# Kernel tuning notes

Measured on AMD Instinct MI355X. Metric: run time of the kernel, lower is better.

## Reference

```python
import jax, jax.numpy as jnp
import numpy as np

V = 30000
Y = 30000
D = 768
B = 8
N = 512
PAD_ID = 0
POS_EXPONENT = 1
NEG_INF = 1e12
LN_EPS = 1e-5


def setup_inputs() -> dict:
    key = jax.random.key(0)
    k1, k2, k3, k4, k5 = jax.random.split(key, 5)
    M_s = jax.random.randint(k1, (B, N), 0, V, dtype=jnp.int64)
    E_v = jax.random.normal(k2, (V, D), dtype=jnp.float32) * 0.02
    E_y = jax.random.normal(k3, (Y, D), dtype=jnp.float32) * 0.02
    # padding_idx=0 -> zero rows
    E_v = E_v.at[PAD_ID].set(0.0)
    E_y = E_y.at[PAD_ID].set(0.0)
    W_A = jax.random.normal(k4, (D, D), dtype=jnp.float32) * (1.0 / np.sqrt(D))
    W_O = jax.random.normal(k5, (D, D), dtype=jnp.float32) * (1.0 / np.sqrt(D))
    gamma = jnp.ones((D,), dtype=jnp.float32)
    beta = jnp.zeros((D,), dtype=jnp.float32)
    return {"M_s": M_s, "E_v": E_v, "E_y": E_y, "W_A": W_A, "W_O": W_O,
            "gamma": gamma, "beta": beta}


def positional_rep(seq_len: int, exponent: int) -> jnp.ndarray:
    idx = jnp.arange(seq_len)
    rel = (idx[None, :] - idx[:, None]).astype(jnp.float32)  # [N, N], j - i
    sign = jnp.where(rel >= 0, 1.0, -1.0)
    return sign * jnp.abs(rel) ** exponent


def layer_norm(x, gamma, beta):
    mu = jnp.mean(x, axis=-1, keepdims=True)
    var = jnp.mean((x - mu) ** 2, axis=-1, keepdims=True)
    return (x - mu) * jax.lax.rsqrt(var + LN_EPS) * gamma + beta


def reference(M_s, E_v, E_y, W_A, W_O, gamma, beta):
    # Embedding lookup (dropout is identity at eval / p=0)
    X = E_v[M_s]                                   # [B, N, D]
    Q = X                                          # self-attention mode (v_q=None)
    mask = (M_s != PAD_ID)                         # [B, N]

    # attention: logits = (Q @ W_A) @ X^T + pos_bias, mask, softmax
    logits = jnp.einsum('bnd,bmd->bnm', Q @ W_A, X)  # [B, N, N]
    logits = logits + positional_rep(X.shape[1], POS_EXPONENT)[None]
    logits = jnp.where(mask[:, None, :], logits, -NEG_INF)
    A = jax.nn.softmax(logits, axis=-1)            # [B, N, N]
    Q_c = jnp.einsum('bnm,bmd->bnd', A, X @ W_O)   # [B, N, D]

    H = layer_norm(Q_c + Q, gamma, beta)           # [B, N, D]
    y_logits = jnp.einsum('bnd,yd->bny', H, E_y)   # [B, N, Y]
    return y_logits, A
```

## Files before the change

kernel.cpp:

```cpp
#include <hip/hip_runtime.h>
#include <hip/hip_bf16.h>

using bf16 = __hip_bfloat16;
typedef __attribute__((ext_vector_type(8))) short bf16x8;
typedef __attribute__((ext_vector_type(4))) float f32x4;

#define DEV __device__ __forceinline__

#define AS1 __attribute__((address_space(1)))
#define AS3 __attribute__((address_space(3)))
#define SB  __builtin_amdgcn_sched_barrier(0)
#define BARR __builtin_amdgcn_s_barrier()
#define LG0 asm volatile("s_waitcnt lgkmcnt(0)" ::: "memory")
#define VM4 asm volatile("s_waitcnt vmcnt(4)" ::: "memory")
#define VM0 asm volatile("s_waitcnt vmcnt(0)" ::: "memory")
#define VM48 asm volatile("s_waitcnt vmcnt(48)" ::: "memory")

static constexpr int Bsz = 8, Nseq = 512, Dm = 768, Vv = 30000, Yv = 30000;
static constexpr int Ypad = 30208;
static constexpr int NTILE = 118;
static constexpr int TT = 16 * NTILE;
static constexpr int Tok = Bsz * Nseq;
static constexpr int NT = Dm / 64;

#define MF16(MQ, NQ, BR)                                                      \
    __builtin_amdgcn_s_setprio(1);                                            \
    _Pragma("unroll") for (int mm = 0; mm < 4; ++mm)                          \
    _Pragma("unroll") for (int nn = 0; nn < 2; ++nn) {                        \
        acc[(MQ)*4+mm][(NQ)*2+nn] = __builtin_amdgcn_mfma_f32_16x16x32_bf16(  \
            afr[mm][0], BR[nn][0], acc[(MQ)*4+mm][(NQ)*2+nn], 0, 0, 0);       \
        acc[(MQ)*4+mm][(NQ)*2+nn] = __builtin_amdgcn_mfma_f32_16x16x32_bf16(  \
            afr[mm][1], BR[nn][1], acc[(MQ)*4+mm][(NQ)*2+nn], 0, 0, 0);       \
    }                                                                         \
    __builtin_amdgcn_s_setprio(0);

__global__ __launch_bounds__(512, 2)
void gemm_big(const bf16* __restrict__ Ag, const bf16* __restrict__ Bg,
              float* __restrict__ Cg, float* __restrict__ dump)
{
    __shared__ bf16 sm[8][8192];

    const int p = blockIdx.x;
    const int tid  = threadIdx.x;
    const int lane = tid & 63;
    const int wid  = tid >> 6;
    const int wm   = wid >> 2;
    const int wn   = wid & 3;

    const int lr = tid >> 3;
    const int sc = ((tid & 7) ^ (lr & 7)) << 3;
    const int ldsOff = wid << 9;

    const int fl = lane & 15;
    const int fh = lane >> 4;
    const int e0 = (fh ^ (fl & 7)) << 3;
    const int aro = (wm * 64 + fl) * 64;
    const int bro = (wn * 32 + fl) * 64;

    bf16x8 afr[4][2], b0r[2][2], b1r[2][2];
    f32x4 acc[8][4] = {};
    float* dmp = dump + (size_t)p * 512 + tid;

#define STAGEP(AP, BP, CI, OP, H, TILE)                                        \
    {                                                                          \
        const bf16* _s = ((OP) ? (BP) : (AP)) + (long)(H) * 128 * Dm + (TILE) * 64;\
        __builtin_amdgcn_global_load_lds((const AS1 void*)_s,                  \
            (AS3 void*)&sm[CI][ldsOff], 16, 0, 0);                             \
        __builtin_amdgcn_global_load_lds((const AS1 void*)(_s + (long)64 * Dm),\
            (AS3 void*)&sm[CI][4096 + ldsOff], 16, 0, 0);                      \
    }
#define STAGE(CI, OP, H, TILE) STAGEP(aS, bS, CI, OP, H, TILE)
#define RDA(CI)                                                                \
    _Pragma("unroll") for (int mm = 0; mm < 4; ++mm) {                         \
        afr[mm][0] = *(const bf16x8*)&sm[CI][aro + mm * 1024 + e0];            \
        afr[mm][1] = *(const bf16x8*)&sm[CI][aro + mm * 1024 + (e0 ^ 32)];     \
    }
#define RDB(BR, CI)                                                            \
    _Pragma("unroll") for (int nn = 0; nn < 2; ++nn) {                         \
        BR[nn][0] = *(const bf16x8*)&sm[CI][bro + nn * 1024 + e0];             \
        BR[nn][1] = *(const bf16x8*)&sm[CI][bro + nn * 1024 + (e0 ^ 32)];      \
    }

    int l = p;
    int s0 = (l & 7) * (TT >> 3) + (l >> 3);
    int mT = s0 & 15, nT = s0 >> 4;
    const bf16* aS = Ag + (long)(mT * 256 + lr) * Dm + sc;
    const bf16* bS = Bg + (long)(nT * 256 + lr) * Dm + sc;

    STAGE(0, 0, 0, 0) STAGE(2, 1, 0, 0) STAGE(3, 1, 1, 0) STAGE(1, 0, 1, 0)
    STAGE(4, 0, 0, 1) STAGE(7, 1, 1, 1)
    VM4; SB; BARR; SB;

#pragma unroll 1
    while (true) {
#pragma unroll 1
        for (int t = 0; t < NT - 2; t += 2) {
            STAGE(6, 1, 0, t + 1)
            RDA(0) RDB(b0r, 2)
            SB; BARR; LG0; SB;
            MF16(0, 0, b0r)
            SB; BARR; SB;
            STAGE(5, 0, 1, t + 1)
            RDB(b1r, 3)
            SB; BARR; LG0; SB;
            MF16(0, 1, b1r)
            SB; BARR; SB;
            STAGE(0, 0, 0, t + 2)
            RDA(1)
            SB; BARR; LG0; SB;
            MF16(1, 1, b1r)
            SB; BARR; SB;
            STAGE(3, 1, 1, t + 2)
            VM4; SB; BARR; SB;
            MF16(1, 0, b0r)
            SB; BARR; SB;
            STAGE(2, 1, 0, t + 2)
            RDA(4) RDB(b0r, 6)
            SB; BARR; LG0; SB;
            MF16(0, 0, b0r)
            SB; BARR; SB;
            STAGE(1, 0, 1, t + 2)
            RDB(b1r, 7)
            SB; BARR; LG0; SB;
            MF16(0, 1, b1r)
            SB; BARR; SB;
            STAGE(4, 0, 0, t + 3)
            RDA(5)
            SB; BARR; LG0; SB;
            MF16(1, 1, b1r)
            SB; BARR; SB;
            STAGE(7, 1, 1, t + 3)
            VM4; SB; BARR; SB;
            MF16(1, 0, b0r)
            SB; BARR; SB;
        }

        {
            const int t = NT - 2;
            STAGE(6, 1, 0, t + 1)
            RDA(0) RDB(b0r, 2)
            SB; BARR; LG0; SB;
            MF16(0, 0, b0r)
            SB; BARR; SB;
            STAGE(5, 0, 1, t + 1)
            RDB(b1r, 3)
            SB; BARR; LG0; SB;
            MF16(0, 1, b1r)
            SB; BARR; SB;
            RDA(1)
            SB; BARR; LG0; SB;
            MF16(1, 1, b1r)
            SB; BARR; SB;
            VM0; SB; BARR; SB;
            MF16(1, 0, b0r)
            SB; BARR; SB;
            RDA(4) RDB(b0r, 6)
            SB; BARR; LG0; SB;
            MF16(0, 0, b0r)
            SB; BARR; SB;
            RDB(b1r, 7)
            SB; BARR; LG0; SB;
            MF16(0, 1, b1r)
            SB; BARR; SB;
            RDA(5)
            SB; BARR; LG0; SB;
            MF16(1, 1, b1r)
            SB; BARR; SB;
            MF16(1, 0, b0r)
        }

        const int l2 = l + 256;
        const bool more = (l2 < TT);
        const int s2 = ((l2 & 7) * (TT >> 3) + (l2 >> 3));
        const int mT2 = s2 & 15, nT2 = s2 >> 4;
        const bf16* aS2 = Ag + (long)(mT2 * 256 + lr) * Dm + sc;
        const bf16* bS2 = Bg + (long)(nT2 * 256 + lr) * Dm + sc;
        if (more) {
            STAGEP(aS2, bS2, 0, 0, 0, 0) STAGEP(aS2, bS2, 2, 1, 0, 0)
            STAGEP(aS2, bS2, 3, 1, 1, 0) STAGEP(aS2, bS2, 1, 0, 1, 0)
            STAGEP(aS2, bS2, 4, 0, 0, 1) STAGEP(aS2, bS2, 7, 1, 1, 1)
            SB;
        }
        {
            const int rB = mT * 256 + wm * 64 + fh * 4;
            const int cB = nT * 256 + wn * 32 + fl;
#pragma unroll
            for (int mq = 0; mq < 2; ++mq)
#pragma unroll
            for (int mm = 0; mm < 4; ++mm)
#pragma unroll
            for (int nq = 0; nq < 2; ++nq)
#pragma unroll
            for (int nn = 0; nn < 2; ++nn) {
                const int c = cB + nq * 128 + nn * 16;
                const int r = rB + mq * 128 + mm * 16;
                const bool ok = (c < Yv);
#pragma unroll
                for (int j = 0; j < 4; ++j) {
                    float* dst = ok ? (Cg + (long)(r + j) * Yv + c) : dmp;
                    *dst = acc[mq * 4 + mm][nq * 2 + nn][j];
                }
            }
        }
#pragma unroll
        for (int i = 0; i < 8; ++i)
#pragma unroll
            for (int n = 0; n < 4; ++n) acc[i][n] = (f32x4){0.f, 0.f, 0.f, 0.f};
        if (!more) break;
        l = l2; mT = mT2; nT = nT2; aS = aS2; bS = bS2;
        SB; VM48; SB; BARR; SB;
    }
#undef STAGEP
#undef STAGE
#undef RDA
#undef RDB
}

template<bool STORE_BF16>
__global__ __launch_bounds__(256)
void gemm_bt(const bf16* __restrict__ Ag, const bf16* __restrict__ Bg,
             void* __restrict__ Cg, int M, int Nc, int K, int lda, int ldc,
             long sA, long sB, long sC)
{
    __shared__ bf16 As[128 * 32];
    __shared__ bf16 Bs[128 * 32];

    const int bz = blockIdx.z;
    const bf16* A  = Ag + (long)bz * sA;
    const bf16* Bm = Bg + (long)bz * sB;

    const int bid = blockIdx.x;
    const int nTilesM = M >> 7;
    const int mTile = bid % nTilesM;
    const int nTile = bid / nTilesM;

    const int tid  = threadIdx.x;
    const int wave = tid >> 6;
    const int lane = tid & 63;

    const int sRow = (wave << 4) + (lane >> 2);
    const int sCol = (lane & 3) << 3;

    const long aBase = (long)(mTile * 128) * lda;
    const long bBase = (long)(nTile * 128) * K;

    const int fl = lane & 15;
    const int fh = lane >> 4;
    const int wRow = (wave >> 1) << 6;
    const int wCol = (wave & 1) << 6;

    f32x4 acc[4][4] = {};

    for (int k0 = 0; k0 < K; k0 += 32) {
#pragma unroll
        for (int t = 0; t < 2; ++t) {
            const bf16* gA = A  + aBase + (long)(t * 64 + sRow) * lda + (k0 + sCol);
            const bf16* gB = Bm + bBase + (long)(t * 64 + sRow) * K + (k0 + sCol);
            bf16* lA = &As[(t * 64 + (wave << 4)) * 32];
            bf16* lB = &Bs[(t * 64 + (wave << 4)) * 32];
            __builtin_amdgcn_global_load_lds(
                (const AS1 void*)gA, (AS3 void*)lA, 16, 0, 0);
            __builtin_amdgcn_global_load_lds(
                (const AS1 void*)gB, (AS3 void*)lB, 16, 0, 0);
        }
        __syncthreads();

        bf16x8 af[4], bfg[4];
#pragma unroll
        for (int m = 0; m < 4; ++m)
            af[m] = *(const bf16x8*)&As[(wRow + m * 16 + fl) * 32 + fh * 8];
#pragma unroll
        for (int n = 0; n < 4; ++n)
            bfg[n] = *(const bf16x8*)&Bs[(wCol + n * 16 + fl) * 32 + fh * 8];
#pragma unroll
        for (int m = 0; m < 4; ++m)
#pragma unroll
            for (int n = 0; n < 4; ++n)
                acc[m][n] = __builtin_amdgcn_mfma_f32_16x16x32_bf16(
                    af[m], bfg[n], acc[m][n], 0, 0, 0);
        __syncthreads();
    }

    const int rBase = mTile * 128 + wRow + fh * 4;
    const int cBase = nTile * 128 + wCol + fl;
#pragma unroll
    for (int m = 0; m < 4; ++m) {
#pragma unroll
        for (int n = 0; n < 4; ++n) {
            int gc = cBase + n * 16;
            int gr = rBase + m * 16;
            if (STORE_BF16) {
                bf16* C = (bf16*)Cg + (long)bz * sC;
#pragma unroll
                for (int j = 0; j < 4; ++j)
                    C[(long)(gr + j) * ldc + gc] = __float2bfloat16(acc[m][n][j]);
            } else {
                float* C = (float*)Cg + (long)bz * sC;
#pragma unroll
                for (int j = 0; j < 4; ++j)
                    C[(long)(gr + j) * ldc + gc] = acc[m][n][j];
            }
        }
    }
}

__global__ __launch_bounds__(192) void k_cvt_ey(const float* __restrict__ Ey,
                                                bf16* __restrict__ Eyb)
{
    int row = blockIdx.x;
    int d = threadIdx.x * 4;
    union { bf16 h[4]; uint2 u; } pk;
    if (row < Yv) {
        float4 v = *(const float4*)(Ey + (long)row * Dm + d);
        pk.h[0] = __float2bfloat16(v.x); pk.h[1] = __float2bfloat16(v.y);
        pk.h[2] = __float2bfloat16(v.z); pk.h[3] = __float2bfloat16(v.w);
    } else {
        pk.h[0] = pk.h[1] = pk.h[2] = pk.h[3] = __float2bfloat16(0.f);
    }
    *(uint2*)(Eyb + (long)row * Dm + d) = pk.u;
}

__global__ void k_wT(const float* __restrict__ WA, const float* __restrict__ WO,
                     bf16* __restrict__ Wcat)
{
    __shared__ float t[32][33];
    const float* W = blockIdx.z ? WO : WA;
    bf16* WT = Wcat + (size_t)blockIdx.z * Dm * Dm;
    int bx = blockIdx.x * 32;
    int by = blockIdx.y * 32;
    int tx = threadIdx.x, ty = threadIdx.y;
#pragma unroll
    for (int i = 0; i < 32; i += 8)
        t[ty + i][tx] = W[(long)(bx + ty + i) * Dm + (by + tx)];
    __syncthreads();
#pragma unroll
    for (int i = 0; i < 32; i += 8)
        WT[(long)(by + ty + i) * Dm + (bx + tx)] = __float2bfloat16(t[tx][ty + i]);
}

__global__ __launch_bounds__(192) void k_gather(const int* __restrict__ Ms,
                                                const float* __restrict__ Ev,
                                                bf16* __restrict__ Xb)
{
    int token = blockIdx.x;
    int id = Ms[token];
    int d = threadIdx.x * 4;
    float4 v = *(const float4*)(Ev + (long)id * Dm + d);
    union { bf16 h[4]; uint2 u; } pk;
    pk.h[0] = __float2bfloat16(v.x); pk.h[1] = __float2bfloat16(v.y);
    pk.h[2] = __float2bfloat16(v.z); pk.h[3] = __float2bfloat16(v.w);
    *(uint2*)(Xb + (long)token * Dm + d) = pk.u;
}

__global__ void k_xwoT(const bf16* __restrict__ Xo, bf16* __restrict__ XoT)
{
    __shared__ bf16 t[32][33];
    int b = blockIdx.z;
    const bf16* src = Xo + (long)b * Nseq * 1536 + 768;
    bf16* dst = XoT + (long)b * Dm * Nseq;
    int bx = blockIdx.x * 32;
    int by = blockIdx.y * 32;
    int tx = threadIdx.x, ty = threadIdx.y;
#pragma unroll
    for (int i = 0; i < 32; i += 8)
        t[ty + i][tx] = src[(long)(bx + ty + i) * 1536 + (by + tx)];
    __syncthreads();
#pragma unroll
    for (int i = 0; i < 32; i += 8)
        dst[(long)(by + ty + i) * Nseq + (bx + tx)] = t[tx][ty + i];
}

DEV float waveMax(float v) {
#pragma unroll
    for (int o = 32; o > 0; o >>= 1) v = fmaxf(v, __shfl_xor(v, o, 64));
    return v;
}
DEV float waveSum(float v) {
#pragma unroll
    for (int o = 32; o > 0; o >>= 1) v += __shfl_xor(v, o, 64);
    return v;
}

__global__ __launch_bounds__(256) void k_softmax(const float* __restrict__ L,
                                                 const int* __restrict__ Ms,
                                                 float* __restrict__ Aout,
                                                 bf16* __restrict__ Ab)
{
    __shared__ float red[8];
    int row = blockIdx.x;
    int b = row >> 9, i = row & 511;
    const float* l = L + (long)row * Nseq;
    const int* ms = Ms + (b << 9);
    int t = threadIdx.x;
    int wid = t >> 6, lane = t & 63;
    int j0 = t, j1 = t + 256;

    float a0 = l[j0] + (float)(j0 - i);
    float a1 = l[j1] + (float)(j1 - i);
    if (ms[j0] == 0) a0 = -1e12f;
    if (ms[j1] == 0) a1 = -1e12f;

    float m = waveMax(fmaxf(a0, a1));
    if (lane == 0) red[wid] = m;
    __syncthreads();
    m = fmaxf(fmaxf(red[0], red[1]), fmaxf(red[2], red[3]));

    float e0 = expf(a0 - m), e1 = expf(a1 - m);
    float s = waveSum(e0 + e1);
    if (lane == 0) red[4 + wid] = s;
    __syncthreads();
    s = red[4] + red[5] + red[6] + red[7];
    float inv = 1.0f / s;

    float r0 = e0 * inv, r1 = e1 * inv;
    Aout[(long)row * Nseq + j0] = r0;
    Aout[(long)row * Nseq + j1] = r1;
    Ab[(long)row * Nseq + j0] = __float2bfloat16(r0);
    Ab[(long)row * Nseq + j1] = __float2bfloat16(r1);
}

__global__ __launch_bounds__(256) void k_ln(const float* __restrict__ Qc,
                                            const int* __restrict__ Ms,
                                            const float* __restrict__ Ev,
                                            const float* __restrict__ gamma,
                                            const float* __restrict__ beta,
                                            bf16* __restrict__ Hb)
{
    __shared__ float red[8];
    int row = blockIdx.x;
    int id = Ms[row];
    const float* q = Qc + (long)row * Dm;
    const float* e = Ev + (long)id * Dm;
    int t = threadIdx.x;
    int wid = t >> 6, lane = t & 63;

    float x[3];
#pragma unroll
    for (int c = 0; c < 3; ++c) x[c] = q[t + c * 256] + e[t + c * 256];

    float s = waveSum(x[0] + x[1] + x[2]);
    if (lane == 0) red[wid] = s;
    __syncthreads();
    float mu = (red[0] + red[1] + red[2] + red[3]) * (1.0f / 768.0f);

    float vs = 0.f;
#pragma unroll
    for (int c = 0; c < 3; ++c) { float d = x[c] - mu; vs += d * d; }
    vs = waveSum(vs);
    if (lane == 0) red[4 + wid] = vs;
    __syncthreads();
    float var = (red[4] + red[5] + red[6] + red[7]) * (1.0f / 768.0f);
    float rstd = rsqrtf(var + 1e-5f);

#pragma unroll
    for (int c = 0; c < 3; ++c) {
        int d = t + c * 256;
        Hb[(long)row * Dm + d] =
            __float2bfloat16((x[c] - mu) * rstd * gamma[d] + beta[d]);
    }
}

extern "C" void kernel_launch(void* const* d_in, const int* in_sizes, int n_in,
                              void* d_out, int out_size, void* d_ws, size_t ws_size,
                              hipStream_t stream)
{
    const int*   Ms    = (const int*)d_in[0];
    const float* Ev    = (const float*)d_in[1];
    const float* Ey    = (const float*)d_in[2];
    const float* WA    = (const float*)d_in[3];
    const float* WO    = (const float*)d_in[4];
    const float* gamma = (const float*)d_in[5];
    const float* beta  = (const float*)d_in[6];

    float* y_out = (float*)d_out;
    float* A_out = y_out + (size_t)Tok * Yv;

    char* ws = (char*)d_ws;
    size_t off = 0;
    auto alloc = [&](size_t n) { char* p = ws + off; off += (n + 255) & ~(size_t)255; return p; };
    bf16*  Xb    = (bf16*) alloc((size_t)Tok * Dm * 2);
    bf16*  WcatT = (bf16*) alloc((size_t)2 * Dm * Dm * 2);
    bf16*  QXWb  = (bf16*) alloc((size_t)Tok * 1536 * 2);
    bf16*  XWobT = (bf16*) alloc((size_t)Tok * Dm * 2);
    float* Lf    = (float*)alloc((size_t)Tok * Nseq * 4);
    bf16*  Ab    = (bf16*) alloc((size_t)Tok * Nseq * 2);
    float* Qc    = (float*)alloc((size_t)Tok * Dm * 4);
    bf16*  Hb    = (bf16*) alloc((size_t)Tok * Dm * 2);
    bf16*  Eyb   = (bf16*) alloc((size_t)Ypad * Dm * 2);
    float* dump  = (float*)alloc((size_t)256 * 512 * 4);

    k_cvt_ey<<<dim3(Ypad), dim3(192), 0, stream>>>(Ey, Eyb);
    k_wT<<<dim3(24, 24, 2), dim3(32, 8), 0, stream>>>(WA, WO, WcatT);
    k_gather<<<dim3(Tok), dim3(192), 0, stream>>>(Ms, Ev, Xb);
    gemm_bt<true><<<dim3(384), dim3(256), 0, stream>>>(
        Xb, WcatT, (void*)QXWb, Tok, 1536, Dm, Dm, 1536, 0L, 0L, 0L);
    gemm_bt<false><<<dim3(16, 1, 8), dim3(256), 0, stream>>>(
        QXWb, Xb, (void*)Lf, Nseq, Nseq, Dm, 1536, Nseq,
        (long)Nseq * 1536, (long)Nseq * Dm, (long)Nseq * Nseq);
    k_softmax<<<dim3(Tok), dim3(256), 0, stream>>>(Lf, Ms, A_out, Ab);
    k_xwoT<<<dim3(16, 24, 8), dim3(32, 8), 0, stream>>>(QXWb, XWobT);
    gemm_bt<false><<<dim3(24, 1, 8), dim3(256), 0, stream>>>(
        Ab, XWobT, (void*)Qc, Nseq, Dm, Nseq, Nseq, Dm,
        (long)Nseq * Nseq, (long)Dm * Nseq, (long)Nseq * Dm);
    k_ln<<<dim3(Tok), dim3(256), 0, stream>>>(Qc, Ms, Ev, gamma, beta, Hb);
    gemm_big<<<dim3(256), dim3(512), 0, stream>>>(Hb, Eyb, y_out, dump);
}
```

Before: 397.9 us.

## Pin A-tile per block in big GEMM, use nontemporal stores, widen Ey conversion

The persistent output GEMM now walks tiles so that each block keeps a fixed M tile (mT constant) and only advances along N. This lets it keep reusing the same A-row addresses and drop the A pointer recomputation. Output logits and softmax probabilities are written with nontemporal stores so the large streaming writes do not evict cached operands. The E_y fp32-to-bf16 conversion kernel now processes 8 elements per thread with nontemporal loads and 16-byte stores over a flat index. The new tile walk changes L2 reuse patterns across blocks and relies on TT being divisible so every block sees the same mT.

```diff
diff --git a/kernel.cpp b/kernel.cpp
--- a/kernel.cpp
+++ b/kernel.cpp
@@ -81,9 +81,9 @@
         BR[nn][1] = *(const bf16x8*)&sm[CI][bro + nn * 1024 + (e0 ^ 32)];      \
     }
 
-    int l = p;
-    int s0 = (l & 7) * (TT >> 3) + (l >> 3);
-    int mT = s0 & 15, nT = s0 >> 4;
+    int s = (p & 7) * 32 + (p >> 3);
+    const int mT = s & 15;
+    int nT = s >> 4;
     const bf16* aS = Ag + (long)(mT * 256 + lr) * Dm + sc;
     const bf16* bS = Bg + (long)(nT * 256 + lr) * Dm + sc;
 
@@ -169,16 +169,14 @@
             MF16(1, 0, b0r)
         }
 
-        const int l2 = l + 256;
-        const bool more = (l2 < TT);
-        const int s2 = ((l2 & 7) * (TT >> 3) + (l2 >> 3));
-        const int mT2 = s2 & 15, nT2 = s2 >> 4;
-        const bf16* aS2 = Ag + (long)(mT2 * 256 + lr) * Dm + sc;
+        const int s2 = s + 256;
+        const bool more = (s2 < TT);
+        const int nT2 = s2 >> 4;
         const bf16* bS2 = Bg + (long)(nT2 * 256 + lr) * Dm + sc;
         if (more) {
-            STAGEP(aS2, bS2, 0, 0, 0, 0) STAGEP(aS2, bS2, 2, 1, 0, 0)
-            STAGEP(aS2, bS2, 3, 1, 1, 0) STAGEP(aS2, bS2, 1, 0, 1, 0)
-            STAGEP(aS2, bS2, 4, 0, 0, 1) STAGEP(aS2, bS2, 7, 1, 1, 1)
+            STAGEP(aS, bS2, 0, 0, 0, 0) STAGEP(aS, bS2, 2, 1, 0, 0)
+            STAGEP(aS, bS2, 3, 1, 1, 0) STAGEP(aS, bS2, 1, 0, 1, 0)
+            STAGEP(aS, bS2, 4, 0, 0, 1) STAGEP(aS, bS2, 7, 1, 1, 1)
             SB;
         }
         {
@@ -198,7 +196,7 @@
 #pragma unroll
                 for (int j = 0; j < 4; ++j) {
                     float* dst = ok ? (Cg + (long)(r + j) * Yv + c) : dmp;
-                    *dst = acc[mq * 4 + mm][nq * 2 + nn][j];
+                    __builtin_nontemporal_store(acc[mq * 4 + mm][nq * 2 + nn][j], dst);
                 }
             }
         }
@@ -207,7 +205,7 @@
 #pragma unroll
             for (int n = 0; n < 4; ++n) acc[i][n] = (f32x4){0.f, 0.f, 0.f, 0.f};
         if (!more) break;
-        l = l2; mT = mT2; nT = nT2; aS = aS2; bS = bS2;
+        s = s2; nT = nT2; bS = bS2;
         SB; VM48; SB; BARR; SB;
     }
 #undef STAGEP
@@ -304,20 +302,26 @@
     }
 }
 
-__global__ __launch_bounds__(192) void k_cvt_ey(const float* __restrict__ Ey,
+__global__ __launch_bounds__(256) void k_cvt_ey(const float* __restrict__ Ey,
                                                 bf16* __restrict__ Eyb)
 {
-    int row = blockIdx.x;
-    int d = threadIdx.x * 4;
-    union { bf16 h[4]; uint2 u; } pk;
+    const long idx = ((long)blockIdx.x * 256 + threadIdx.x) * 8;
+    const int row = (int)(idx / Dm);
+    union { bf16 h[8]; uint4 u; } pk;
     if (row < Yv) {
-        float4 v = *(const float4*)(Ey + (long)row * Dm + d);
-        pk.h[0] = __float2bfloat16(v.x); pk.h[1] = __float2bfloat16(v.y);
-        pk.h[2] = __float2bfloat16(v.z); pk.h[3] = __float2bfloat16(v.w);
+        const f32x4* s = (const f32x4*)(Ey + idx);
+        f32x4 a = __builtin_nontemporal_load(s);
+        f32x4 b = __builtin_nontemporal_load(s + 1);
+#pragma unroll
+        for (int i = 0; i < 4; ++i) {
+            pk.h[i]     = __float2bfloat16(a[i]);
+            pk.h[4 + i] = __float2bfloat16(b[i]);
+        }
     } else {
-        pk.h[0] = pk.h[1] = pk.h[2] = pk.h[3] = __float2bfloat16(0.f);
-    }
-    *(uint2*)(Eyb + (long)row * Dm + d) = pk.u;
+#pragma unroll
+        for (int i = 0; i < 8; ++i) pk.h[i] = __float2bfloat16(0.f);
+    }
+    *(uint4*)(Eyb + idx) = pk.u;
 }
 
 __global__ void k_wT(const float* __restrict__ WA, const float* __restrict__ WO,
@@ -413,8 +417,8 @@
     float inv = 1.0f / s;
 
     float r0 = e0 * inv, r1 = e1 * inv;
-    Aout[(long)row * Nseq + j0] = r0;
-    Aout[(long)row * Nseq + j1] = r1;
+    __builtin_nontemporal_store(r0, &Aout[(long)row * Nseq + j0]);
+    __builtin_nontemporal_store(r1, &Aout[(long)row * Nseq + j1]);
     Ab[(long)row * Nseq + j0] = __float2bfloat16(r0);
     Ab[(long)row * Nseq + j1] = __float2bfloat16(r1);
 }
@@ -489,7 +493,7 @@
     bf16*  Eyb   = (bf16*) alloc((size_t)Ypad * Dm * 2);
     float* dump  = (float*)alloc((size_t)256 * 512 * 4);
 
-    k_cvt_ey<<<dim3(Ypad), dim3(192), 0, stream>>>(Ey, Eyb);
+    k_cvt_ey<<<dim3(11328), dim3(256), 0, stream>>>(Ey, Eyb);
     k_wT<<<dim3(24, 24, 2), dim3(32, 8), 0, stream>>>(WA, WO, WcatT);
     k_gather<<<dim3(Tok), dim3(192), 0, stream>>>(Ms, Ev, Xb);
     gemm_bt<true><<<dim3(384), dim3(256), 0, stream>>>(
```

Result: faster. 371.8 us (-6.6%).
